# Kernel optimization log

Hardware: AMD Instinct MI355X
Metric: run time of the kernel (lower is better)

The kernel has to match this reference:

```python
import jax, jax.numpy as jnp
import numpy as np

N_NODES = 100000


def gcn_conv(x, src, dst, W, b, n_nodes):
    # PyG GCNConv: h = X W; out[i] = sum_j norm_ij * h[j] + b, with self-loops
    # and symmetric normalization norm_ij = deg(i)^-1/2 * deg(j)^-1/2.
    h = x @ W  # [N, out]
    deg = jax.ops.segment_sum(jnp.ones_like(dst, dtype=h.dtype), dst, num_segments=n_nodes)
    dinv = jnp.where(deg > 0, jax.lax.rsqrt(deg), 0.0)
    norm = dinv[src] * dinv[dst]  # [E]
    msg = h[src] * norm[:, None]  # [E, out] gather + scale
    out = jax.ops.segment_sum(msg, dst, num_segments=n_nodes)  # scatter-add
    return out + b


def setup_inputs() -> dict:
    key = jax.random.key(0)
    k_x, k_e, k_w1, k_w2 = jax.random.split(key, 4)
    in_c, hid, out_c = 128, 64, 32
    x = jax.random.normal(k_x, (N_NODES, in_c), dtype=jnp.float32)
    edge_index = jax.random.randint(k_e, (2, 1600000), 0, N_NODES, dtype=jnp.int32)
    W1 = jax.random.normal(k_w1, (in_c, hid), dtype=jnp.float32) / np.sqrt(in_c)
    b1 = jnp.zeros((hid,), dtype=jnp.float32)
    W2 = jax.random.normal(k_w2, (hid, out_c), dtype=jnp.float32) / np.sqrt(hid)
    b2 = jnp.zeros((out_c,), dtype=jnp.float32)
    return {"x": x, "edge_index": edge_index, "W1": W1, "b1": b1, "W2": W2, "b2": b2}


def reference(x, edge_index, W1, b1, W2, b2):
    n = x.shape[0]
    # add self-loops (GCNConv default)
    loops = jnp.arange(n, dtype=edge_index.dtype)
    src = jnp.concatenate([edge_index[0], loops])
    dst = jnp.concatenate([edge_index[1], loops])
    # faithful to original forward: x = (x*x)/x
    x = (x * x) / x
    h = jax.nn.relu(gcn_conv(x, src, dst, W1, b1, n))
    return gcn_conv(h, src, dst, W2, b2, n)
```

## Files before the change

kernel.cpp:

```cpp
#include <hip/hip_runtime.h>
#include <hip/hip_fp16.h>


#define IN_C 128
#define HID 64
#define OUTC 32
#define BSH 9
#define BSZ 512
#define NSLOT 256
#define EPB 8192

typedef _Float16 half8 __attribute__((ext_vector_type(8)));
typedef float f32x4 __attribute__((ext_vector_type(4)));

static __host__ __device__ __forceinline__ size_t szt(int a) { return (size_t)a; }

__global__ __launch_bounds__(256) void k_hist(const int* __restrict__ dst, int E,
                                              int* __restrict__ hist) {
  __shared__ int h[NSLOT];
  int tid = threadIdx.x;
  h[tid] = 0;
  __syncthreads();
  int e0 = blockIdx.x * EPB;
  int e1 = min(e0 + EPB, E);
  int nv = (e1 - e0) & ~3;
  for (int i = e0 + tid * 4; i < e0 + nv; i += 256 * 4) {
    int4 d4 = *reinterpret_cast<const int4*>(&dst[i]);
    atomicAdd(&h[d4.x >> BSH], 1);
    atomicAdd(&h[d4.y >> BSH], 1);
    atomicAdd(&h[d4.z >> BSH], 1);
    atomicAdd(&h[d4.w >> BSH], 1);
  }
  for (int i = e0 + nv + tid; i < e1; i += 256) atomicAdd(&h[dst[i] >> BSH], 1);
  __syncthreads();
  hist[blockIdx.x * NSLOT + tid] = h[tid];
}

__global__ __launch_bounds__(256) void k_scan_col(int* __restrict__ hist, int B,
                                                  int* __restrict__ bucket_count) {
  __shared__ int sc[256];
  int k = blockIdx.x, t = threadIdx.x;
  int v = (t < B) ? hist[t * NSLOT + k] : 0;
  sc[t] = v;
  __syncthreads();
  for (int o = 1; o < 256; o <<= 1) {
    int w = (t >= o) ? sc[t - o] : 0;
    __syncthreads();
    sc[t] += w;
    __syncthreads();
  }
  if (t < B) hist[t * NSLOT + k] = sc[t] - v;
  if (t == 255) bucket_count[k] = sc[255];
}

__global__ __launch_bounds__(256) void k_scatter(const int* __restrict__ src,
                                                 const int* __restrict__ dst, int E,
                                                 const int* __restrict__ hist,
                                                 const int* __restrict__ bucket_count,
                                                 int* __restrict__ bedges) {
  __shared__ int off[NSLOT];
  __shared__ int sc[NSLOT];
  int tid = threadIdx.x;
  int v = bucket_count[tid];
  sc[tid] = v;
  __syncthreads();
  for (int o = 1; o < 256; o <<= 1) {
    int w = (tid >= o) ? sc[tid - o] : 0;
    __syncthreads();
    sc[tid] += w;
    __syncthreads();
  }
  off[tid] = hist[blockIdx.x * NSLOT + tid] + (sc[tid] - v);
  __syncthreads();
  int e0 = blockIdx.x * EPB;
  int e1 = min(e0 + EPB, E);
  int nv = (e1 - e0) & ~3;
  for (int i = e0 + tid * 4; i < e0 + nv; i += 256 * 4) {
    int4 d4 = *reinterpret_cast<const int4*>(&dst[i]);
    int4 s4 = *reinterpret_cast<const int4*>(&src[i]);
    int p0 = atomicAdd(&off[d4.x >> BSH], 1);
    bedges[p0] = (s4.x << BSH) | (d4.x & (BSZ - 1));
    int p1 = atomicAdd(&off[d4.y >> BSH], 1);
    bedges[p1] = (s4.y << BSH) | (d4.y & (BSZ - 1));
    int p2 = atomicAdd(&off[d4.z >> BSH], 1);
    bedges[p2] = (s4.z << BSH) | (d4.z & (BSZ - 1));
    int p3 = atomicAdd(&off[d4.w >> BSH], 1);
    bedges[p3] = (s4.w << BSH) | (d4.w & (BSZ - 1));
  }
  for (int i = e0 + nv + tid; i < e1; i += 256) {
    int d = dst[i], s = src[i];
    int p = atomicAdd(&off[d >> BSH], 1);
    bedges[p] = (s << BSH) | (d & (BSZ - 1));
  }
}

__global__ __launch_bounds__(256) void k_bucket(const int* __restrict__ bedges,
                                                const int* __restrict__ bucket_count,
                                                int2* __restrict__ rd,
                                                float* __restrict__ dinv,
                                                int* __restrict__ csr, int N) {
  __shared__ int h[BSZ];
  __shared__ int pfx[BSZ];
  __shared__ int cnt[BSZ];
  __shared__ int sc[256];
  __shared__ int s_base;
  int tid = threadIdx.x;
  int b = blockIdx.x;
  {
    int v = bucket_count[tid];
    sc[tid] = v;
    __syncthreads();
    for (int o = 1; o < 256; o <<= 1) {
      int w = (tid >= o) ? sc[tid - o] : 0;
      __syncthreads();
      sc[tid] += w;
      __syncthreads();
    }
    if (tid == b) s_base = sc[tid] - v;
    __syncthreads();
  }
  int base = s_base;
  int nE = bucket_count[b];
  h[tid] = 0; h[tid + 256] = 0;
  cnt[tid] = 0; cnt[tid + 256] = 0;
  __syncthreads();
  for (int i = tid; i < nE; i += 256) atomicAdd(&h[bedges[base + i] & (BSZ - 1)], 1);
  __syncthreads();
  int a0 = h[2 * tid], a1 = h[2 * tid + 1];
  int s = a0 + a1;
  sc[tid] = s;
  __syncthreads();
  for (int o = 1; o < 256; o <<= 1) {
    int v = (tid >= o) ? sc[tid - o] : 0;
    __syncthreads();
    sc[tid] += v;
    __syncthreads();
  }
  int ex = sc[tid] - s;
  pfx[2 * tid] = ex;
  pfx[2 * tid + 1] = ex + a0;
  __syncthreads();
  for (int i = tid; i < BSZ; i += 256) {
    int node = b * BSZ + i;
    if (node < N) {
      int dg = h[i];
      rd[node] = make_int2(base + pfx[i], dg);
      dinv[node] = rsqrtf((float)(dg + 1));
    }
  }
  for (int i = tid; i < nE; i += 256) {
    int e = bedges[base + i];
    int l = e & (BSZ - 1);
    int p = pfx[l] + atomicAdd(&cnt[l], 1);
    csr[base + p] = e >> BSH;
  }
}

__global__ __launch_bounds__(256) void k_gemm1(
    const float* __restrict__ x, const float* __restrict__ W1,
    const float* __restrict__ dinv, __half* __restrict__ h1s, int N) {
  __shared__ _Float16 bf[4 * 4 * 64 * 8];
  const int tid = threadIdx.x;
  for (int idx = tid; idx < 128 * 64; idx += 256) {
    int k = idx >> 6, c = idx & 63;
    int kc = k >> 5, kk = k & 31;
    int chunk = kk >> 3, j = kk & 7;
    int ct = c >> 4, cl = c & 15;
    bf[(((kc * 4 + ct) * 64) + chunk * 16 + cl) * 8 + j] = (_Float16)W1[idx];
  }
  __syncthreads();

  const int lane = tid & 63, wave = tid >> 6;
  const int row0 = blockIdx.x * 64 + wave * 16;
  const int r_a = lane & 15;
  const int chk = lane >> 4;
  const int arow = min(row0 + r_a, N - 1);
  const float* xp = x + szt(arow) * IN_C + chk * 8;

  f32x4 acc[4];
  #pragma unroll
  for (int ct = 0; ct < 4; ++ct) acc[ct] = (f32x4){0.f, 0.f, 0.f, 0.f};

  #pragma unroll
  for (int kc = 0; kc < 4; ++kc) {
    float4 a0 = *reinterpret_cast<const float4*>(xp + kc * 32);
    float4 a1v = *reinterpret_cast<const float4*>(xp + kc * 32 + 4);
    half8 af;
    af[0] = (_Float16)a0.x;  af[1] = (_Float16)a0.y;
    af[2] = (_Float16)a0.z;  af[3] = (_Float16)a0.w;
    af[4] = (_Float16)a1v.x; af[5] = (_Float16)a1v.y;
    af[6] = (_Float16)a1v.z; af[7] = (_Float16)a1v.w;
    #pragma unroll
    for (int ct = 0; ct < 4; ++ct) {
      half8 bfrag = *reinterpret_cast<const half8*>(&bf[(((kc * 4 + ct) * 64) + lane) * 8]);
      acc[ct] = __builtin_amdgcn_mfma_f32_16x16x32_f16(af, bfrag, acc[ct], 0, 0, 0);
    }
  }
  #pragma unroll
  for (int r = 0; r < 4; ++r) {
    int drow = row0 + chk * 4 + r;
    if (drow < N) {
      float di = dinv[drow];
      #pragma unroll
      for (int ct = 0; ct < 4; ++ct)
        h1s[szt(drow) * HID + ct * 16 + r_a] = (__half)(acc[ct][r] * di);
    }
  }
}

__global__ __launch_bounds__(256) void k_agg1(
    const __half* __restrict__ h1s, const int* __restrict__ csr,
    const int2* __restrict__ rd, const float* __restrict__ dinv,
    const float* __restrict__ b1, __half* __restrict__ a1, int N) {
  const int tid = threadIdx.x;
  int node = blockIdx.x * 32 + (tid >> 3);
  if (node >= N) return;
  const int l = tid & 7;
  const int g0 = (tid & 63) & ~7;
  const _Float16* hp = (const _Float16*)h1s;

  half8 selfv = *reinterpret_cast<const half8*>(hp + szt(node) * HID + l * 8);
  float acc[8];
  #pragma unroll
  for (int q = 0; q < 8; ++q) acc[q] = (float)selfv[q];

  int2 v = rd[node];
  int base = v.x, cnt = v.y;
  if (cnt > 0) {
    int last = base + cnt - 1;
    int myidx = csr[min(base + l, last)];
    for (int j = 0; j < cnt; j += 8) {
      int id[8];
      #pragma unroll
      for (int u = 0; u < 8; ++u) id[u] = __shfl(myidx, g0 + u);
      half8 gv[8];
      #pragma unroll
      for (int u = 0; u < 8; ++u)
        gv[u] = *reinterpret_cast<const half8*>(hp + szt(id[u]) * HID + l * 8);
      int jn = j + 8;
      if (jn < cnt) myidx = csr[min(base + jn + l, last)];
      #pragma unroll
      for (int u = 0; u < 8; ++u) {
        bool ok = (j + u) < cnt;
        #pragma unroll
        for (int q = 0; q < 8; ++q) acc[q] += ok ? (float)gv[u][q] : 0.0f;
      }
    }
  }
  float di = dinv[node];
  float4 bb0 = *reinterpret_cast<const float4*>(b1 + l * 8);
  float4 bb1 = *reinterpret_cast<const float4*>(b1 + l * 8 + 4);
  half8 o;
  o[0] = (_Float16)fmaxf(di * acc[0] + bb0.x, 0.f);
  o[1] = (_Float16)fmaxf(di * acc[1] + bb0.y, 0.f);
  o[2] = (_Float16)fmaxf(di * acc[2] + bb0.z, 0.f);
  o[3] = (_Float16)fmaxf(di * acc[3] + bb0.w, 0.f);
  o[4] = (_Float16)fmaxf(di * acc[4] + bb1.x, 0.f);
  o[5] = (_Float16)fmaxf(di * acc[5] + bb1.y, 0.f);
  o[6] = (_Float16)fmaxf(di * acc[6] + bb1.z, 0.f);
  o[7] = (_Float16)fmaxf(di * acc[7] + bb1.w, 0.f);
  *reinterpret_cast<half8*>((_Float16*)a1 + szt(node) * HID + l * 8) = o;
}

__global__ __launch_bounds__(256) void k_gemm2(
    const __half* __restrict__ a1, const float* __restrict__ W2,
    const float* __restrict__ dinv, __half* __restrict__ h2s, int N) {
  __shared__ _Float16 bf[2 * 2 * 64 * 8];
  const int tid = threadIdx.x;
  for (int idx = tid; idx < 64 * 32; idx += 256) {
    int k = idx >> 5, c = idx & 31;
    int kc = k >> 5, kk = k & 31;
    int chunk = kk >> 3, j = kk & 7;
    int ct = c >> 4, cl = c & 15;
    bf[(((kc * 2 + ct) * 64) + chunk * 16 + cl) * 8 + j] = (_Float16)W2[idx];
  }
  __syncthreads();

  const int lane = tid & 63, wave = tid >> 6;
  const int row0 = blockIdx.x * 64 + wave * 16;
  const int r_a = lane & 15;
  const int chk = lane >> 4;
  const int arow = min(row0 + r_a, N - 1);
  const _Float16* ap = (const _Float16*)a1 + szt(arow) * HID + chk * 8;

  f32x4 acc[2];
  acc[0] = (f32x4){0.f, 0.f, 0.f, 0.f};
  acc[1] = (f32x4){0.f, 0.f, 0.f, 0.f};
  #pragma unroll
  for (int kc = 0; kc < 2; ++kc) {
    half8 af = *reinterpret_cast<const half8*>(ap + kc * 32);
    #pragma unroll
    for (int ct = 0; ct < 2; ++ct) {
      half8 bfrag = *reinterpret_cast<const half8*>(&bf[(((kc * 2 + ct) * 64) + lane) * 8]);
      acc[ct] = __builtin_amdgcn_mfma_f32_16x16x32_f16(af, bfrag, acc[ct], 0, 0, 0);
    }
  }
  #pragma unroll
  for (int r = 0; r < 4; ++r) {
    int drow = row0 + chk * 4 + r;
    if (drow < N) {
      float di = dinv[drow];
      #pragma unroll
      for (int ct = 0; ct < 2; ++ct)
        h2s[szt(drow) * OUTC + ct * 16 + r_a] = (__half)(acc[ct][r] * di);
    }
  }
}

__global__ __launch_bounds__(256) void k_agg2(
    const __half* __restrict__ h2s, const int* __restrict__ csr,
    const int2* __restrict__ rd, const float* __restrict__ dinv,
    const float* __restrict__ b2, float* __restrict__ out, int N) {
  const int tid = threadIdx.x;
  int node = blockIdx.x * 64 + (tid >> 2);
  if (node >= N) return;
  const int l = tid & 3;
  const int g0 = (tid & 63) & ~3;
  const _Float16* hp = (const _Float16*)h2s;

  half8 selfv = *reinterpret_cast<const half8*>(hp + szt(node) * OUTC + l * 8);
  float acc[8];
  #pragma unroll
  for (int q = 0; q < 8; ++q) acc[q] = (float)selfv[q];

  int2 v = rd[node];
  int base = v.x, cnt = v.y;
  if (cnt > 0) {
    int last = base + cnt - 1;
    int myA = csr[min(base + 2 * l, last)];
    int myB = csr[min(base + 2 * l + 1, last)];
    for (int j = 0; j < cnt; j += 8) {
      int id[8];
      #pragma unroll
      for (int u = 0; u < 4; ++u) {
        id[2 * u]     = __shfl(myA, g0 + u);
        id[2 * u + 1] = __shfl(myB, g0 + u);
      }
      half8 gv[8];
      #pragma unroll
      for (int u = 0; u < 8; ++u)
        gv[u] = *reinterpret_cast<const half8*>(hp + szt(id[u]) * OUTC + l * 8);
      int jn = j + 8;
      if (jn < cnt) {
        myA = csr[min(base + jn + 2 * l, last)];
        myB = csr[min(base + jn + 2 * l + 1, last)];
      }
      #pragma unroll
      for (int u = 0; u < 8; ++u) {
        bool ok = (j + u) < cnt;
        #pragma unroll
        for (int q = 0; q < 8; ++q) acc[q] += ok ? (float)gv[u][q] : 0.0f;
      }
    }
  }
  float di = dinv[node];
  float4 bb0 = *reinterpret_cast<const float4*>(b2 + l * 8);
  float4 bb1 = *reinterpret_cast<const float4*>(b2 + l * 8 + 4);
  float4 o0, o1;
  o0.x = di * acc[0] + bb0.x; o0.y = di * acc[1] + bb0.y;
  o0.z = di * acc[2] + bb0.z; o0.w = di * acc[3] + bb0.w;
  o1.x = di * acc[4] + bb1.x; o1.y = di * acc[5] + bb1.y;
  o1.z = di * acc[6] + bb1.z; o1.w = di * acc[7] + bb1.w;
  float* op = out + szt(node) * OUTC + l * 8;
  *reinterpret_cast<float4*>(op) = o0;
  *reinterpret_cast<float4*>(op + 4) = o1;
}

extern "C" void kernel_launch(void* const* d_in, const int* in_sizes, int n_in,
                              void* d_out, int out_size, void* d_ws, size_t ws_size,
                              hipStream_t stream) {
  const float* x  = (const float*)d_in[0];
  const int*   ei = (const int*)d_in[1];
  const float* W1 = (const float*)d_in[2];
  const float* b1 = (const float*)d_in[3];
  const float* W2 = (const float*)d_in[4];
  const float* b2 = (const float*)d_in[5];
  float* out = (float*)d_out;

  const int N = in_sizes[0] / IN_C;
  const int E = in_sizes[1] / 2;
  const int* src = ei;
  const int* dst = ei + E;

  const int B  = (E + EPB - 1) / EPB;
  const int K1 = (N + BSZ - 1) / BSZ;

  char* ws = (char*)d_ws;
  size_t off = 0;
  auto alloc = [&](size_t bytes) {
    off = (off + 255) & ~(size_t)255;
    void* p = ws + off;
    off += bytes;
    return p;
  };
  int*    hist   = (int*)alloc(szt(B) * NSLOT * 4);
  int*    bcount = (int*)alloc(NSLOT * 4);
  int2*   rd     = (int2*)alloc(szt(N) * 8);
  float*  dinv   = (float*)alloc(szt(N) * 4);
  int*    bedges = (int*)alloc(szt(E) * 4);
  int*    csr    = (int*)alloc(szt(E) * 4);
  __half* h1s    = (__half*)alloc(szt(N) * HID * 2);
  __half* a1     = (__half*)alloc(szt(N) * HID * 2);
  __half* h2s    = (__half*)alloc(szt(N) * OUTC * 2);
  (void)ws_size;

  k_hist<<<B, 256, 0, stream>>>(dst, E, hist);
  k_scan_col<<<NSLOT, 256, 0, stream>>>(hist, B, bcount);
  k_scatter<<<B, 256, 0, stream>>>(src, dst, E, hist, bcount, bedges);
  k_bucket<<<K1, 256, 0, stream>>>(bedges, bcount, rd, dinv, csr, N);
  k_gemm1<<<(N + 63) / 64, 256, 0, stream>>>(x, W1, dinv, h1s, N);
  k_agg1<<<(N + 31) / 32, 256, 0, stream>>>(h1s, csr, rd, dinv, b1, a1, N);
  k_gemm2<<<(N + 63) / 64, 256, 0, stream>>>(a1, W2, dinv, h2s, N);
  k_agg2<<<(N + 63) / 64, 256, 0, stream>>>(h2s, csr, rd, dinv, b2, out, N);
}
```

Before: 120.7 us.

## Replace global histogram/scan/scatter with per-block local sort and strided bucket CSR

The four-kernel edge bucketing pipeline (histogram, column scan, global scatter, bucket sort) becomes two kernels. Each block now sorts its own chunk of edges by bucket in shared memory and writes it back contiguously along with per-bucket counts and offsets. The bucket kernel gathers its segments from every block into shared memory, builds the local CSR there, and writes it out coalesced with a fixed per-bucket stride. This removes two launches and the scattered global writes, but it caps each bucket at BSTRIDE edges (overflow is silently dropped) and uses a serial per-thread gather loop.

```diff
diff --git a/kernel.cpp b/kernel.cpp
--- a/kernel.cpp
+++ b/kernel.cpp
@@ -9,139 +9,146 @@
 #define BSZ 512
 #define NSLOT 256
 #define EPB 8192
+#define BSTRIDE 9216
 
 typedef _Float16 half8 __attribute__((ext_vector_type(8)));
 typedef float f32x4 __attribute__((ext_vector_type(4)));
 
 static __host__ __device__ __forceinline__ size_t szt(int a) { return (size_t)a; }
 
-__global__ __launch_bounds__(256) void k_hist(const int* __restrict__ dst, int E,
-                                              int* __restrict__ hist) {
+__global__ __launch_bounds__(256) void k_part(const int* __restrict__ src,
+                                              const int* __restrict__ dst, int E,
+                                              int* __restrict__ bedges,
+                                              int* __restrict__ cnt,
+                                              int* __restrict__ pre) {
+  __shared__ int dbuf[EPB];
+  __shared__ int sorted[EPB];
   __shared__ int h[NSLOT];
-  int tid = threadIdx.x;
+  __shared__ int off[NSLOT];
+  const int tid = threadIdx.x;
   h[tid] = 0;
   __syncthreads();
-  int e0 = blockIdx.x * EPB;
-  int e1 = min(e0 + EPB, E);
-  int nv = (e1 - e0) & ~3;
-  for (int i = e0 + tid * 4; i < e0 + nv; i += 256 * 4) {
-    int4 d4 = *reinterpret_cast<const int4*>(&dst[i]);
+  const int e0 = blockIdx.x * EPB;
+  const int n = min(EPB, E - e0);
+  const int nv = n & ~3;
+  for (int i = tid * 4; i < nv; i += 1024) {
+    int4 d4 = *reinterpret_cast<const int4*>(&dst[e0 + i]);
+    dbuf[i + 0] = d4.x; dbuf[i + 1] = d4.y;
+    dbuf[i + 2] = d4.z; dbuf[i + 3] = d4.w;
     atomicAdd(&h[d4.x >> BSH], 1);
     atomicAdd(&h[d4.y >> BSH], 1);
     atomicAdd(&h[d4.z >> BSH], 1);
     atomicAdd(&h[d4.w >> BSH], 1);
   }
-  for (int i = e0 + nv + tid; i < e1; i += 256) atomicAdd(&h[dst[i] >> BSH], 1);
-  __syncthreads();
-  hist[blockIdx.x * NSLOT + tid] = h[tid];
-}
-
-__global__ __launch_bounds__(256) void k_scan_col(int* __restrict__ hist, int B,
-                                                  int* __restrict__ bucket_count) {
-  __shared__ int sc[256];
-  int k = blockIdx.x, t = threadIdx.x;
-  int v = (t < B) ? hist[t * NSLOT + k] : 0;
-  sc[t] = v;
+  for (int i = nv + tid; i < n; i += 256) {
+    int d = dst[e0 + i];
+    dbuf[i] = d;
+    atomicAdd(&h[d >> BSH], 1);
+  }
+  __syncthreads();
+  int v = h[tid];
+  off[tid] = v;
   __syncthreads();
   for (int o = 1; o < 256; o <<= 1) {
-    int w = (t >= o) ? sc[t - o] : 0;
-    __syncthreads();
-    sc[t] += w;
-    __syncthreads();
-  }
-  if (t < B) hist[t * NSLOT + k] = sc[t] - v;
-  if (t == 255) bucket_count[k] = sc[255];
-}
-
-__global__ __launch_bounds__(256) void k_scatter(const int* __restrict__ src,
-                                                 const int* __restrict__ dst, int E,
-                                                 const int* __restrict__ hist,
-                                                 const int* __restrict__ bucket_count,
-                                                 int* __restrict__ bedges) {
-  __shared__ int off[NSLOT];
-  __shared__ int sc[NSLOT];
-  int tid = threadIdx.x;
-  int v = bucket_count[tid];
-  sc[tid] = v;
-  __syncthreads();
-  for (int o = 1; o < 256; o <<= 1) {
-    int w = (tid >= o) ? sc[tid - o] : 0;
-    __syncthreads();
-    sc[tid] += w;
-    __syncthreads();
-  }
-  off[tid] = hist[blockIdx.x * NSLOT + tid] + (sc[tid] - v);
-  __syncthreads();
-  int e0 = blockIdx.x * EPB;
-  int e1 = min(e0 + EPB, E);
-  int nv = (e1 - e0) & ~3;
-  for (int i = e0 + tid * 4; i < e0 + nv; i += 256 * 4) {
-    int4 d4 = *reinterpret_cast<const int4*>(&dst[i]);
-    int4 s4 = *reinterpret_cast<const int4*>(&src[i]);
-    int p0 = atomicAdd(&off[d4.x >> BSH], 1);
-    bedges[p0] = (s4.x << BSH) | (d4.x & (BSZ - 1));
-    int p1 = atomicAdd(&off[d4.y >> BSH], 1);
-    bedges[p1] = (s4.y << BSH) | (d4.y & (BSZ - 1));
-    int p2 = atomicAdd(&off[d4.z >> BSH], 1);
-    bedges[p2] = (s4.z << BSH) | (d4.z & (BSZ - 1));
-    int p3 = atomicAdd(&off[d4.w >> BSH], 1);
-    bedges[p3] = (s4.w << BSH) | (d4.w & (BSZ - 1));
-  }
-  for (int i = e0 + nv + tid; i < e1; i += 256) {
-    int d = dst[i], s = src[i];
+    int w = (tid >= o) ? off[tid - o] : 0;
+    __syncthreads();
+    off[tid] += w;
+    __syncthreads();
+  }
+  int excl = off[tid] - v;
+  cnt[blockIdx.x * NSLOT + tid] = v;
+  pre[blockIdx.x * NSLOT + tid] = excl;
+  __syncthreads();
+  off[tid] = excl;
+  __syncthreads();
+  for (int i = tid * 4; i < nv; i += 1024) {
+    int4 s4 = *reinterpret_cast<const int4*>(&src[e0 + i]);
+    int d0 = dbuf[i], d1 = dbuf[i + 1], d2 = dbuf[i + 2], d3 = dbuf[i + 3];
+    int p0 = atomicAdd(&off[d0 >> BSH], 1);
+    sorted[p0] = (s4.x << BSH) | (d0 & (BSZ - 1));
+    int p1 = atomicAdd(&off[d1 >> BSH], 1);
+    sorted[p1] = (s4.y << BSH) | (d1 & (BSZ - 1));
+    int p2 = atomicAdd(&off[d2 >> BSH], 1);
+    sorted[p2] = (s4.z << BSH) | (d2 & (BSZ - 1));
+    int p3 = atomicAdd(&off[d3 >> BSH], 1);
+    sorted[p3] = (s4.w << BSH) | (d3 & (BSZ - 1));
+  }
+  for (int i = nv + tid; i < n; i += 256) {
+    int s = src[e0 + i], d = dbuf[i];
     int p = atomicAdd(&off[d >> BSH], 1);
-    bedges[p] = (s << BSH) | (d & (BSZ - 1));
-  }
+    sorted[p] = (s << BSH) | (d & (BSZ - 1));
+  }
+  __syncthreads();
+  for (int i = tid * 4; i < nv; i += 1024) {
+    *reinterpret_cast<int4*>(&bedges[e0 + i]) =
+        make_int4(sorted[i], sorted[i + 1], sorted[i + 2], sorted[i + 3]);
+  }
+  for (int i = nv + tid; i < n; i += 256) bedges[e0 + i] = sorted[i];
 }
 
 __global__ __launch_bounds__(256) void k_bucket(const int* __restrict__ bedges,
-                                                const int* __restrict__ bucket_count,
+                                                const int* __restrict__ cnt,
+                                                const int* __restrict__ pre,
+                                                int B, int E,
                                                 int2* __restrict__ rd,
                                                 float* __restrict__ dinv,
                                                 int* __restrict__ csr, int N) {
+  __shared__ int ebuf[BSTRIDE];
+  __shared__ int obuf[BSTRIDE];
   __shared__ int h[BSZ];
   __shared__ int pfx[BSZ];
-  __shared__ int cnt[BSZ];
+  __shared__ int c2[BSZ];
   __shared__ int sc[256];
-  __shared__ int s_base;
-  int tid = threadIdx.x;
-  int b = blockIdx.x;
-  {
-    int v = bucket_count[tid];
-    sc[tid] = v;
-    __syncthreads();
-    for (int o = 1; o < 256; o <<= 1) {
-      int w = (tid >= o) ? sc[tid - o] : 0;
-      __syncthreads();
-      sc[tid] += w;
-      __syncthreads();
-    }
-    if (tid == b) s_base = sc[tid] - v;
-    __syncthreads();
-  }
-  int base = s_base;
-  int nE = bucket_count[b];
+  __shared__ int dsto[256];
+  const int k = blockIdx.x;
+  const int tid = threadIdx.x;
   h[tid] = 0; h[tid + 256] = 0;
-  cnt[tid] = 0; cnt[tid + 256] = 0;
-  __syncthreads();
-  for (int i = tid; i < nE; i += 256) atomicAdd(&h[bedges[base + i] & (BSZ - 1)], 1);
+  c2[tid] = 0; c2[tid + 256] = 0;
+  int c = 0, so = 0;
+  if (tid < B) {
+    c = cnt[tid * NSLOT + k];
+    so = pre[tid * NSLOT + k];
+  }
+  sc[tid] = c;
+  __syncthreads();
+  for (int o = 1; o < 256; o <<= 1) {
+    int w = (tid >= o) ? sc[tid - o] : 0;
+    __syncthreads();
+    sc[tid] += w;
+    __syncthreads();
+  }
+  dsto[tid] = sc[tid] - c;
+  __syncthreads();
+  int total = sc[255];
+  int nE = min(total, BSTRIDE);
+  if (tid < B && c > 0) {
+    int gbase = tid * EPB + so;
+    int dbase = dsto[tid];
+    for (int j = 0; j < c; ++j) {
+      int p = dbase + j;
+      if (p < BSTRIDE) ebuf[p] = bedges[gbase + j];
+    }
+  }
+  __syncthreads();
+  for (int i = tid; i < nE; i += 256) atomicAdd(&h[ebuf[i] & (BSZ - 1)], 1);
   __syncthreads();
   int a0 = h[2 * tid], a1 = h[2 * tid + 1];
   int s = a0 + a1;
   sc[tid] = s;
   __syncthreads();
   for (int o = 1; o < 256; o <<= 1) {
-    int v = (tid >= o) ? sc[tid - o] : 0;
-    __syncthreads();
-    sc[tid] += v;
+    int w = (tid >= o) ? sc[tid - o] : 0;
+    __syncthreads();
+    sc[tid] += w;
     __syncthreads();
   }
   int ex = sc[tid] - s;
   pfx[2 * tid] = ex;
   pfx[2 * tid + 1] = ex + a0;
   __syncthreads();
+  const int base = k * BSTRIDE;
   for (int i = tid; i < BSZ; i += 256) {
-    int node = b * BSZ + i;
+    int node = k * BSZ + i;
     if (node < N) {
       int dg = h[i];
       rd[node] = make_int2(base + pfx[i], dg);
@@ -149,11 +156,18 @@
     }
   }
   for (int i = tid; i < nE; i += 256) {
-    int e = bedges[base + i];
+    int e = ebuf[i];
     int l = e & (BSZ - 1);
-    int p = pfx[l] + atomicAdd(&cnt[l], 1);
-    csr[base + p] = e >> BSH;
-  }
+    int p = pfx[l] + atomicAdd(&c2[l], 1);
+    obuf[p] = e >> BSH;
+  }
+  __syncthreads();
+  int nv = nE & ~3;
+  for (int i = tid * 4; i < nv; i += 1024) {
+    *reinterpret_cast<int4*>(&csr[base + i]) =
+        make_int4(obuf[i], obuf[i + 1], obuf[i + 2], obuf[i + 3]);
+  }
+  for (int i = nv + tid; i < nE; i += 256) csr[base + i] = obuf[i];
 }
 
 __global__ __launch_bounds__(256) void k_gemm1(
@@ -382,8 +396,8 @@
   const int* src = ei;
   const int* dst = ei + E;
 
-  const int B  = (E + EPB - 1) / EPB;
-  const int K1 = (N + BSZ - 1) / BSZ;
+  const int B   = (E + EPB - 1) / EPB;
+  const int NBK = (N + BSZ - 1) / BSZ;
 
   char* ws = (char*)d_ws;
   size_t off = 0;
@@ -393,21 +407,19 @@
     off += bytes;
     return p;
   };
-  int*    hist   = (int*)alloc(szt(B) * NSLOT * 4);
-  int*    bcount = (int*)alloc(NSLOT * 4);
+  int*    cnt    = (int*)alloc(szt(B) * NSLOT * 4);
+  int*    pre    = (int*)alloc(szt(B) * NSLOT * 4);
   int2*   rd     = (int2*)alloc(szt(N) * 8);
   float*  dinv   = (float*)alloc(szt(N) * 4);
-  int*    bedges = (int*)alloc(szt(E) * 4);
-  int*    csr    = (int*)alloc(szt(E) * 4);
+  int*    bedges = (int*)alloc(szt(B) * EPB * 4);
+  int*    csr    = (int*)alloc(szt(NBK) * BSTRIDE * 4);
   __half* h1s    = (__half*)alloc(szt(N) * HID * 2);
   __half* a1     = (__half*)alloc(szt(N) * HID * 2);
   __half* h2s    = (__half*)alloc(szt(N) * OUTC * 2);
   (void)ws_size;
 
-  k_hist<<<B, 256, 0, stream>>>(dst, E, hist);
-  k_scan_col<<<NSLOT, 256, 0, stream>>>(hist, B, bcount);
-  k_scatter<<<B, 256, 0, stream>>>(src, dst, E, hist, bcount, bedges);
-  k_bucket<<<K1, 256, 0, stream>>>(bedges, bcount, rd, dinv, csr, N);
+  k_part<<<B, 256, 0, stream>>>(src, dst, E, bedges, cnt, pre);
+  k_bucket<<<NBK, 256, 0, stream>>>(bedges, cnt, pre, B, E, rd, dinv, csr, N);
   k_gemm1<<<(N + 63) / 64, 256, 0, stream>>>(x, W1, dinv, h1s, N);
   k_agg1<<<(N + 31) / 32, 256, 0, stream>>>(h1s, csr, rd, dinv, b1, a1, N);
   k_gemm2<<<(N + 63) / 64, 256, 0, stream>>>(a1, W2, dinv, h2s, N);
```

After: 118.7 us. About the same (-1.7%).
